# Kernel tuning notes

Hardware: AMD Instinct MI355X
Metric: run time of the kernel (lower is better)

## Reference

```python
import jax, jax.numpy as jnp
import numpy as np

B, H, W = 4, 128, 128
D_MODEL = 256
N_LAYERS = 4
N_STATE = 64


def _s4d_kernel(log_dt, logA_re, A_im, C_re, C_im, L):
    """S4D (diagonal SSM) convolution kernel of length L. Shapes: log_dt (d,), others (d,N). Returns (d, L)."""
    dt = jnp.exp(log_dt)                       # (d,)
    A = -jnp.exp(logA_re) + 1j * A_im          # (d,N) complex, Re<0 for stability
    C = C_re + 1j * C_im                       # (d,N)
    dtA = dt[:, None] * A                      # (d,N)
    # ZOH-style input matrix folded into C (S4D-Lin):  C * (exp(dt*A)-1)/A
    CB = C * (jnp.exp(dtA) - 1.0) / A          # (d,N)
    pows = jnp.exp(dtA[:, :, None] * jnp.arange(L, dtype=jnp.float32))  # (d,N,L)
    K = jnp.einsum('dn,dnl->dl', CB, pows)     # (d,L) complex
    return 2.0 * K.real


def _layernorm(x, w, b, eps=1e-5):
    mu = jnp.mean(x, axis=-1, keepdims=True)
    var = jnp.mean(jnp.square(x - mu), axis=-1, keepdims=True)
    return (x - mu) * jax.lax.rsqrt(var + eps) * w + b


def setup_inputs() -> dict:
    key = jax.random.key(0)
    ks = jax.random.split(key, 16)
    d, L, N = D_MODEL, N_LAYERS, N_STATE
    x = jax.random.normal(ks[0], (B, H, W, 1), dtype=jnp.float32)
    grid = jax.random.uniform(ks[1], (B, H, W, 1), dtype=jnp.float32)
    W_enc = jax.random.normal(ks[2], (2, d), dtype=jnp.float32) / np.sqrt(2.0)
    b_enc = jnp.zeros((d,), jnp.float32)
    # per-layer, per-axis (axis 0 = H-kernel, axis 1 = W-kernel) SSM params
    log_dt = jax.random.uniform(ks[3], (L, 2, d), jnp.float32,
                                minval=float(np.log(1e-3)), maxval=float(np.log(1e-1)))
    logA_re = jnp.full((L, 2, d, N), float(np.log(0.5)), jnp.float32)
    A_im = jnp.broadcast_to(np.pi * jnp.arange(N, dtype=jnp.float32), (L, 2, d, N)).copy()
    C_re = jax.random.normal(ks[4], (L, 2, d, N), jnp.float32) * float(0.5 ** 0.5)
    C_im = jax.random.normal(ks[5], (L, 2, d, N), jnp.float32) * float(0.5 ** 0.5)
    Dskip = jax.random.normal(ks[6], (L, d), jnp.float32)
    W_out = jax.random.normal(ks[7], (L, d, 2 * d), jnp.float32) / np.sqrt(d)
    b_out = jnp.zeros((L, 2 * d), jnp.float32)
    ln_w = jnp.ones((L, d), jnp.float32)
    ln_b = jnp.zeros((L, d), jnp.float32)
    W_dec = jax.random.normal(ks[8], (d, 1), jnp.float32) / np.sqrt(d)
    b_dec = jnp.zeros((1,), jnp.float32)
    return dict(x=x, grid=grid, W_enc=W_enc, b_enc=b_enc, log_dt=log_dt,
                logA_re=logA_re, A_im=A_im, C_re=C_re, C_im=C_im, Dskip=Dskip,
                W_out=W_out, b_out=b_out, ln_w=ln_w, ln_b=ln_b, W_dec=W_dec, b_dec=b_dec)


def reference(x, grid, W_enc, b_enc, log_dt, logA_re, A_im, C_re, C_im,
              Dskip, W_out, b_out, ln_w, ln_b, W_dec, b_dec):
    # encoder: concat grid, project to d_model  -> (B,H,W,d)
    h = jnp.concatenate([x, grid], axis=-1) @ W_enc + b_enc
    n_fft = (2 * H, 2 * W)
    for i in range(N_LAYERS):
        z = h
        # separable 2D S4ND kernel: outer product of per-axis S4D kernels
        kh = _s4d_kernel(log_dt[i, 0], logA_re[i, 0], A_im[i, 0], C_re[i, 0], C_im[i, 0], H)  # (d,H)
        kw = _s4d_kernel(log_dt[i, 1], logA_re[i, 1], A_im[i, 1], C_re[i, 1], C_im[i, 1], W)  # (d,W)
        K2 = kh[:, :, None] * kw[:, None, :]                     # (d,H,W)
        u = jnp.transpose(z, (0, 3, 1, 2))                       # (B,d,H,W)
        yf = jnp.fft.rfft2(u, s=n_fft) * jnp.fft.rfft2(K2, s=n_fft)
        y = jnp.fft.irfft2(yf, s=n_fft)[..., :H, :W]             # causal 2D conv via zero-pad FFT
        y = y + u * Dskip[i][:, None, None]                      # skip connection D*u
        y = jnp.transpose(y, (0, 2, 3, 1))                       # back to (B,H,W,d)
        y = jax.nn.gelu(y)
        y = y @ W_out[i] + b_out[i]                              # (B,H,W,2d)
        a, g = jnp.split(y, 2, axis=-1)
        y = a * jax.nn.sigmoid(g)                                # GLU output linear
        h = y + h                                                # residual (dropout=0, eval)
        h = _layernorm(h, ln_w[i], ln_b[i])                      # post-norm (prenorm=False)
    return h @ W_dec + b_dec                                     # (B,H,W,1)
```

## Files before the change

kernel.cpp:

```cpp
#include <hip/hip_runtime.h>
#include <math.h>

#define DM 256
#define NS 64
#define SP 128

typedef __attribute__((ext_vector_type(8))) short bf16x8;
typedef __attribute__((ext_vector_type(4))) float f32x4;

__device__ __forceinline__ float gelu_f(float x) {
    float x3 = x * x * x;
    return 0.5f * x * (1.0f + tanhf(0.7978845608028654f * (x + 0.044715f * x3)));
}
__device__ __forceinline__ float sigmoid_f(float x) {
    return 1.0f / (1.0f + expf(-x));
}
__device__ __forceinline__ unsigned short f2bf(float f) {
    unsigned u = __float_as_uint(f);
    u += 0x7fff + ((u >> 16) & 1);
    return (unsigned short)(u >> 16);
}
__device__ __forceinline__ float bf2f(unsigned short b) {
    return __uint_as_float(((unsigned)b) << 16);
}

__global__ __launch_bounds__(128) void gen_k_kernel(
        const float* __restrict__ log_dt, const float* __restrict__ logA_re,
        const float* __restrict__ A_im,   const float* __restrict__ C_re,
        const float* __restrict__ C_im,   float* __restrict__ Kd) {
    int blk = blockIdx.x;
    int d  = blk & (DM - 1);
    int la = blk >> 8;
    int q  = threadIdx.x;
    __shared__ float s_cbr[NS], s_cbi[NS], s_dr[NS], s_di[NS];
    int pbase = (la * DM + d) * NS;
    float dt = expf(log_dt[la * DM + d]);
    if (q < NS) {
        int n = q;
        float ar = -expf(logA_re[pbase + n]);
        float ai = A_im[pbase + n];
        float dr = dt * ar, di = dt * ai;
        float er = expf(dr);
        float sn, cs;
        sincosf(di, &sn, &cs);
        float nr = er * cs - 1.0f, ni = er * sn;
        float inv = 1.0f / (ar * ar + ai * ai);
        float br = (nr * ar + ni * ai) * inv;
        float bi = (ni * ar - nr * ai) * inv;
        float cr = C_re[pbase + n], ci = C_im[pbase + n];
        s_cbr[n] = cr * br - ci * bi;
        s_cbi[n] = cr * bi + ci * br;
        s_dr[n] = dr;
        s_di[n] = di;
    }
    __syncthreads();
    float fq = (float)q;
    float acc = 0.0f;
    for (int n = 0; n < NS; ++n) {
        float pr = expf(s_dr[n] * fq);
        float sn, cs;
        sincosf(s_di[n] * fq, &sn, &cs);
        acc += s_cbr[n] * (pr * cs) - s_cbi[n] * (pr * sn);
    }
    Kd[((size_t)la * DM + d) * SP + q] = 2.0f * acc;
}

__global__ __launch_bounds__(256) void toep_kernel(
        const float* __restrict__ Kd, unsigned short* __restrict__ Tp, int l) {
    int blk = blockIdx.x;
    int axis = blk >> 8, d = blk & 255;
    int la = l * 2 + axis;
    __shared__ float kt[SP];
    if (threadIdx.x < SP) kt[threadIdx.x] = Kd[((size_t)la * DM + d) * SP + threadIdx.x];
    __syncthreads();
    size_t bse = ((size_t)axis * DM + d) * 16384;
    for (int e = threadIdx.x; e < 16384; e += 256) {
        int i = e >> 7, j = e & 127;
        Tp[bse + e] = (j <= i) ? f2bf(kt[i - j]) : (unsigned short)0;
    }
}

__global__ __launch_bounds__(256) void prep_b_kernel(
        const float* __restrict__ Wo, unsigned short* __restrict__ Bt) {
    int idx = blockIdx.x * 256 + threadIdx.x;
    int l = idx >> 17, rem = idx & 131071, n = rem >> 8, k = rem & 255;
    Bt[idx] = f2bf(Wo[(size_t)l * 131072 + k * 512 + n]);
}

__global__ __launch_bounds__(256) void encode_kernel(
        const float* __restrict__ x, const float* __restrict__ g,
        const float* __restrict__ W_enc, const float* __restrict__ b_enc,
        unsigned short* __restrict__ h) {
    int total = 4 * SP * SP * 128;
    for (int idx = blockIdx.x * blockDim.x + threadIdx.x; idx < total;
         idx += gridDim.x * blockDim.x) {
        int c = (idx & 127) * 2;
        int pos = idx >> 7;
        float xv = x[pos], gv = g[pos];
        float v0 = xv * W_enc[c] + gv * W_enc[DM + c] + b_enc[c];
        float v1 = xv * W_enc[c + 1] + gv * W_enc[DM + c + 1] + b_enc[c + 1];
        unsigned o = (unsigned)f2bf(v0) | ((unsigned)f2bf(v1) << 16);
        *(unsigned*)(h + (size_t)pos * DM + c) = o;
    }
}

template <int FUSE>
__global__ __launch_bounds__(256) void transpose_kernel(
        const unsigned short* __restrict__ in, unsigned short* __restrict__ out,
        int Ci, int Ri, int ctmask, int ctshift,
        const unsigned short* __restrict__ hres, const float* __restrict__ Dsk) {
    __shared__ unsigned tile[64][65];
    int bid = blockIdx.x;
    int rt = bid >> ctshift, ct = bid & ctmask;
    int r0 = rt << 6, c0 = ct << 6;
    int tid = threadIdx.x;
    #pragma unroll
    for (int rep = 0; rep < 2; ++rep) {
        int e = rep * 256 + tid;
        int p = e >> 3, cc = e & 7;
        uint4 v = *(const uint4*)(in + (size_t)(r0 + p) * Ci + c0 + cc * 8);
        const unsigned short* pv = (const unsigned short*)&v;
        #pragma unroll
        for (int q = 0; q < 8; ++q) tile[p][cc * 8 + q] = pv[q];
    }
    __syncthreads();
    #pragma unroll
    for (int rep = 0; rep < 2; ++rep) {
        int e = rep * 256 + tid;
        int cc = e >> 3, pc = e & 7;
        unsigned short tmp[8];
        #pragma unroll
        for (int q = 0; q < 8; ++q) tmp[q] = (unsigned short)tile[pc * 8 + q][cc];
        size_t oaddr = (size_t)(c0 + cc) * Ri + r0 + pc * 8;
        if (FUSE) {
            int d0 = r0 + pc * 8;
            uint4 hv = *(const uint4*)(hres + oaddr);
            const unsigned short* hvp = (const unsigned short*)&hv;
            float4 dk0 = *(const float4*)(Dsk + d0);
            float4 dk1 = *(const float4*)(Dsk + d0 + 4);
            #pragma unroll
            for (int q = 0; q < 8; ++q) {
                float dk = (q < 4) ? (&dk0.x)[q] : (&dk1.x)[q - 4];
                float z = fmaf(bf2f(hvp[q]), dk, bf2f(tmp[q]));
                tmp[q] = f2bf(gelu_f(z));
            }
        }
        *(uint4*)(out + oaddr) = *(const uint4*)tmp;
    }
}

__global__ __launch_bounds__(512, 4) void conv_kernel(
        const unsigned short* __restrict__ hc, const unsigned short* __restrict__ Tp,
        unsigned short* __restrict__ Zc) {
    __shared__ unsigned short Tile[128][128];
    __shared__ unsigned short TpL[128][128];
    int bid = blockIdx.x;
    int work = (bid & 7) * 128 + (bid >> 3);
    int d = work >> 2, b = work & 3;
    int tid = threadIdx.x;
    int lane = tid & 63, wv = tid >> 6;
    int lc = lane & 15, g = lane >> 4;

    const unsigned short* TpW = Tp + (size_t)(DM + d) * 16384;
    const unsigned short* TpH = Tp + (size_t)d * 16384;

    {
        const uint4* srcU = (const uint4*)(hc + ((size_t)d * 4 + b) * 16384);
        const uint4* srcT = (const uint4*)TpW;
        #pragma unroll
        for (int it = 0; it < 4; ++it) {
            int e = it * 512 + tid;
            int r = e >> 4, wc = e & 15;
            *(uint4*)&Tile[r][((wc ^ (r & 7)) << 3)] = srcU[e];
            *(uint4*)&TpL[r][((wc ^ (r & 7)) << 3)] = srcT[e];
        }
    }
    __syncthreads();

    f32x4 acc[8];
    #pragma unroll
    for (int ni = 0; ni < 8; ++ni) acc[ni] = (f32x4){0.f, 0.f, 0.f, 0.f};
    #pragma unroll
    for (int kk = 0; kk < 4; ++kk) {
        int hh = wv * 16 + lc;
        bf16x8 a = *(const bf16x8*)&Tile[hh][(((kk * 4 + g) ^ (hh & 7)) << 3)];
        #pragma unroll
        for (int ni = 0; ni < 8; ++ni) {
            int n = ni * 16 + lc;
            bf16x8 bf = *(const bf16x8*)&TpL[n][(((kk * 4 + g) ^ (n & 7)) << 3)];
            acc[ni] = __builtin_amdgcn_mfma_f32_16x16x32_bf16(a, bf, acc[ni], 0, 0, 0);
        }
    }
    __syncthreads();

    {
        int hh0 = wv * 16 + g * 4;
        #pragma unroll
        for (int ni = 0; ni < 8; ++ni) {
            int w = ni * 16 + lc;
            ushort4 p;
            p.x = f2bf(acc[ni][0]); p.y = f2bf(acc[ni][1]);
            p.z = f2bf(acc[ni][2]); p.w = f2bf(acc[ni][3]);
            *(ushort4*)&Tile[w][((((hh0 >> 3) ^ (w & 7)) << 3) | (hh0 & 7))] = p;
        }
        const uint4* srcT = (const uint4*)TpH;
        #pragma unroll
        for (int it = 0; it < 4; ++it) {
            int e = it * 512 + tid;
            int r = e >> 4, wc = e & 15;
            *(uint4*)&TpL[r][((wc ^ (r & 7)) << 3)] = srcT[e];
        }
    }
    __syncthreads();

    #pragma unroll
    for (int ni = 0; ni < 8; ++ni) acc[ni] = (f32x4){0.f, 0.f, 0.f, 0.f};
    #pragma unroll
    for (int kk = 0; kk < 4; ++kk) {
        int w = wv * 16 + lc;
        bf16x8 a = *(const bf16x8*)&Tile[w][(((kk * 4 + g) ^ (w & 7)) << 3)];
        #pragma unroll
        for (int ni = 0; ni < 8; ++ni) {
            int n = ni * 16 + lc;
            bf16x8 bf = *(const bf16x8*)&TpL[n][(((kk * 4 + g) ^ (n & 7)) << 3)];
            acc[ni] = __builtin_amdgcn_mfma_f32_16x16x32_bf16(a, bf, acc[ni], 0, 0, 0);
        }
    }
    __syncthreads();

    {
        int w0 = wv * 16 + g * 4;
        #pragma unroll
        for (int ni = 0; ni < 8; ++ni) {
            int hh = ni * 16 + lc;
            ushort4 p;
            p.x = f2bf(acc[ni][0]); p.y = f2bf(acc[ni][1]);
            p.z = f2bf(acc[ni][2]); p.w = f2bf(acc[ni][3]);
            *(ushort4*)&Tile[hh][((((w0 >> 3) ^ (hh & 7)) << 3) | (w0 & 7))] = p;
        }
    }
    __syncthreads();
    {
        uint4* dst = (uint4*)(Zc + ((size_t)d * 4 + b) * 16384);
        #pragma unroll
        for (int it = 0; it < 4; ++it) {
            int e = it * 512 + tid;
            int r = e >> 4, wc = e & 15;
            dst[e] = *(const uint4*)&Tile[r][((wc ^ (r & 7)) << 3)];
        }
    }
}

__global__ __launch_bounds__(512, 4) void glu_kernel(
        const unsigned short* __restrict__ Ab, const unsigned short* __restrict__ Bt,
        unsigned short* __restrict__ h, const float* __restrict__ bo) {
    __shared__ unsigned short Ba[64][256];
    __shared__ unsigned short Bg[64][256];
    int tid = threadIdx.x;
    int lane = tid & 63, wv = tid >> 6;
    int lc = lane & 15, g = lane >> 4;
    int mb = blockIdx.x & 127;
    int qp = blockIdx.x >> 7;

    {
        const uint4* srcA = (const uint4*)(Bt + (size_t)(qp * 64) * DM);
        const uint4* srcG = (const uint4*)(Bt + (size_t)(256 + qp * 64) * DM);
        #pragma unroll
        for (int it = 0; it < 4; ++it) {
            int e = it * 512 + tid;
            int r = e >> 5, wc = e & 31;
            *(uint4*)&Ba[r][((wc ^ (r & 7)) << 3)] = srcA[e];
            *(uint4*)&Bg[r][((wc ^ (r & 7)) << 3)] = srcG[e];
        }
    }
    __syncthreads();

    #pragma unroll
    for (int s4 = 0; s4 < 4; ++s4) {
        int mrow = mb * 512 + s4 * 128 + wv * 16 + lc;
        bf16x8 af[8];
        #pragma unroll
        for (int kk = 0; kk < 8; ++kk)
            af[kk] = *(const bf16x8*)(Ab + (size_t)mrow * DM + kk * 32 + g * 8);

        f32x4 aa[4], ag[4];
        #pragma unroll
        for (int ni = 0; ni < 4; ++ni) {
            aa[ni] = (f32x4){0.f, 0.f, 0.f, 0.f};
            ag[ni] = (f32x4){0.f, 0.f, 0.f, 0.f};
        }
        #pragma unroll
        for (int kk = 0; kk < 8; ++kk) {
            #pragma unroll
            for (int ni = 0; ni < 4; ++ni) {
                int r = ni * 16 + lc;
                int ch = (((kk * 4 + g) ^ (r & 7)) << 3);
                bf16x8 bfa = *(const bf16x8*)&Ba[r][ch];
                bf16x8 bfg = *(const bf16x8*)&Bg[r][ch];
                aa[ni] = __builtin_amdgcn_mfma_f32_16x16x32_bf16(bfa, af[kk], aa[ni], 0, 0, 0);
                ag[ni] = __builtin_amdgcn_mfma_f32_16x16x32_bf16(bfg, af[kk], ag[ni], 0, 0, 0);
            }
        }

        #pragma unroll
        for (int ni = 0; ni < 4; ++ni) {
            int ca = qp * 64 + ni * 16 + g * 4;
            float4 bav = *(const float4*)(bo + ca);
            float4 bgv = *(const float4*)(bo + 256 + ca);
            size_t pbase = (size_t)mrow * DM + ca;
            uint2 hv = *(const uint2*)(h + pbase);
            float hr[4];
            hr[0] = __uint_as_float(hv.x << 16);
            hr[1] = __uint_as_float(hv.x & 0xffff0000u);
            hr[2] = __uint_as_float(hv.y << 16);
            hr[3] = __uint_as_float(hv.y & 0xffff0000u);
            float o[4];
            #pragma unroll
            for (int reg = 0; reg < 4; ++reg)
                o[reg] = (aa[ni][reg] + (&bav.x)[reg]) * sigmoid_f(ag[ni][reg] + (&bgv.x)[reg]) + hr[reg];
            uint2 ov;
            ov.x = (unsigned)f2bf(o[0]) | ((unsigned)f2bf(o[1]) << 16);
            ov.y = (unsigned)f2bf(o[2]) | ((unsigned)f2bf(o[3]) << 16);
            *(uint2*)(h + pbase) = ov;
        }
    }
}

__global__ __launch_bounds__(256) void ln_tr_kernel(
        unsigned short* __restrict__ hio, unsigned short* __restrict__ hc,
        const float* __restrict__ lnw, const float* __restrict__ lnb) {
    __shared__ unsigned tile[64][65];
    __shared__ float rs[64][2];
    int r0 = blockIdx.x * 64;
    int tid = threadIdx.x;
    int wv = tid >> 6, lane = tid & 63;

    for (int it = 0; it < 16; ++it) {
        int p = it * 4 + wv;
        size_t base = (size_t)(r0 + p) * DM + lane * 4;
        uint2 hv = *(const uint2*)(hio + base);
        float v0 = __uint_as_float(hv.x << 16);
        float v1 = __uint_as_float(hv.x & 0xffff0000u);
        float v2 = __uint_as_float(hv.y << 16);
        float v3 = __uint_as_float(hv.y & 0xffff0000u);
        float s1 = v0 + v1 + v2 + v3;
        float s2 = v0 * v0 + v1 * v1 + v2 * v2 + v3 * v3;
        #pragma unroll
        for (int off = 1; off < 64; off <<= 1) {
            s1 += __shfl_xor(s1, off);
            s2 += __shfl_xor(s2, off);
        }
        if (lane == 0) {
            float mean = s1 * (1.0f / 256.0f);
            float var = s2 * (1.0f / 256.0f) - mean * mean;
            rs[p][0] = mean;
            rs[p][1] = rsqrtf(var + 1e-5f);
        }
    }
    __syncthreads();

    for (int ct = 0; ct < 4; ++ct) {
        int c0 = ct * 64;
        #pragma unroll
        for (int rep = 0; rep < 2; ++rep) {
            int e = rep * 256 + tid;
            int p = e >> 3, cc = e & 7;
            size_t addr = (size_t)(r0 + p) * DM + c0 + cc * 8;
            uint4 v = *(const uint4*)(hio + addr);
            const unsigned short* vp = (const unsigned short*)&v;
            float mn = rs[p][0], iv = rs[p][1];
            int cb = c0 + cc * 8;
            float4 w0 = *(const float4*)(lnw + cb);
            float4 w1 = *(const float4*)(lnw + cb + 4);
            float4 b0 = *(const float4*)(lnb + cb);
            float4 b1 = *(const float4*)(lnb + cb + 4);
            unsigned short tmp[8];
            #pragma unroll
            for (int q = 0; q < 8; ++q) {
                float lw = (q < 4) ? (&w0.x)[q] : (&w1.x)[q - 4];
                float lb = (q < 4) ? (&b0.x)[q] : (&b1.x)[q - 4];
                tmp[q] = f2bf((bf2f(vp[q]) - mn) * iv * lw + lb);
            }
            *(uint4*)(hio + addr) = *(const uint4*)tmp;
            #pragma unroll
            for (int q = 0; q < 8; ++q) tile[p][cc * 8 + q] = tmp[q];
        }
        __syncthreads();
        #pragma unroll
        for (int rep = 0; rep < 2; ++rep) {
            int e = rep * 256 + tid;
            int cc = e >> 3, pc = e & 7;
            unsigned short tmp[8];
            #pragma unroll
            for (int q = 0; q < 8; ++q) tmp[q] = (unsigned short)tile[pc * 8 + q][cc];
            *(uint4*)(hc + (size_t)(c0 + cc) * 65536 + r0 + pc * 8) = *(const uint4*)tmp;
        }
        __syncthreads();
    }
}

__global__ __launch_bounds__(256) void decode_kernel(
        const unsigned short* __restrict__ h, const float* __restrict__ Wd,
        const float* __restrict__ bd, float* __restrict__ out) {
    int pos = blockIdx.x * 4 + (threadIdx.x >> 6);
    int lane = threadIdx.x & 63;
    float s = 0.0f;
    #pragma unroll
    for (int j = 0; j < 4; ++j) {
        int d = j * 64 + lane;
        s += bf2f(h[(size_t)pos * DM + d]) * Wd[d];
    }
    #pragma unroll
    for (int off = 32; off > 0; off >>= 1) s += __shfl_down(s, off);
    if (lane == 0) out[pos] = s + bd[0];
}

extern "C" void kernel_launch(void* const* d_in, const int* in_sizes, int n_in,
                              void* d_out, int out_size, void* d_ws, size_t ws_size,
                              hipStream_t stream) {
    const float* x       = (const float*)d_in[0];
    const float* grid    = (const float*)d_in[1];
    const float* W_enc   = (const float*)d_in[2];
    const float* b_enc   = (const float*)d_in[3];
    const float* log_dt  = (const float*)d_in[4];
    const float* logA_re = (const float*)d_in[5];
    const float* A_im    = (const float*)d_in[6];
    const float* C_re    = (const float*)d_in[7];
    const float* C_im    = (const float*)d_in[8];
    const float* Dskip   = (const float*)d_in[9];
    const float* W_out   = (const float*)d_in[10];
    const float* b_out   = (const float*)d_in[11];
    const float* ln_w    = (const float*)d_in[12];
    const float* ln_b    = (const float*)d_in[13];
    const float* W_dec   = (const float*)d_in[14];
    const float* b_dec   = (const float*)d_in[15];

    char* base = (char*)d_ws;
    float*          Kd  = (float*)base;
    unsigned short* Bt  = (unsigned short*)(base + 1048576);
    unsigned short* hP  = (unsigned short*)(base + 2097152);
    unsigned short* R1  = (unsigned short*)(base + 35651584);
    unsigned short* R2  = (unsigned short*)(base + 69206016);
    unsigned short* Tp  = (unsigned short*)(base + 102760448);

    gen_k_kernel<<<dim3(8 * DM), dim3(128), 0, stream>>>(log_dt, logA_re, A_im,
                                                         C_re, C_im, Kd);
    prep_b_kernel<<<dim3(2048), dim3(256), 0, stream>>>(W_out, Bt);
    encode_kernel<<<dim3(2048), dim3(256), 0, stream>>>(x, grid, W_enc, b_enc, hP);
    transpose_kernel<0><<<dim3(4096), dim3(256), 0, stream>>>(
        hP, R1, 256, 65536, 3, 2, (const unsigned short*)nullptr, (const float*)nullptr);

    for (int l = 0; l < 4; ++l) {
        toep_kernel<<<dim3(512), dim3(256), 0, stream>>>(Kd, Tp, l);
        conv_kernel<<<dim3(1024), dim3(512), 0, stream>>>(R1, Tp, R2);
        transpose_kernel<1><<<dim3(4096), dim3(256), 0, stream>>>(
            R2, R1, 65536, 256, 1023, 10, hP, Dskip + (size_t)l * DM);
        glu_kernel<<<dim3(512), dim3(512), 0, stream>>>(R1,
            Bt + (size_t)l * 131072, hP, b_out + (size_t)l * 512);
        ln_tr_kernel<<<dim3(1024), dim3(256), 0, stream>>>(hP, R1,
            ln_w + (size_t)l * DM, ln_b + (size_t)l * DM);
    }

    decode_kernel<<<dim3(16384), dim3(256), 0, stream>>>(hP, W_dec, b_dec,
                                                         (float*)d_out);
}
```

Baseline: 533.3 us.

## Build Toeplitz tiles in-kernel from Kd and skip last-layer transposed write

Measured after the change: 524.4 us. About the same (-1.7%).

```diff
diff --git a/kernel.cpp b/kernel.cpp
--- a/kernel.cpp
+++ b/kernel.cpp
@@ -65,21 +65,6 @@
     Kd[((size_t)la * DM + d) * SP + q] = 2.0f * acc;
 }
 
-__global__ __launch_bounds__(256) void toep_kernel(
-        const float* __restrict__ Kd, unsigned short* __restrict__ Tp, int l) {
-    int blk = blockIdx.x;
-    int axis = blk >> 8, d = blk & 255;
-    int la = l * 2 + axis;
-    __shared__ float kt[SP];
-    if (threadIdx.x < SP) kt[threadIdx.x] = Kd[((size_t)la * DM + d) * SP + threadIdx.x];
-    __syncthreads();
-    size_t bse = ((size_t)axis * DM + d) * 16384;
-    for (int e = threadIdx.x; e < 16384; e += 256) {
-        int i = e >> 7, j = e & 127;
-        Tp[bse + e] = (j <= i) ? f2bf(kt[i - j]) : (unsigned short)0;
-    }
-}
-
 __global__ __launch_bounds__(256) void prep_b_kernel(
         const float* __restrict__ Wo, unsigned short* __restrict__ Bt) {
     int idx = blockIdx.x * 256 + threadIdx.x;
@@ -150,10 +135,11 @@
 }
 
 __global__ __launch_bounds__(512, 4) void conv_kernel(
-        const unsigned short* __restrict__ hc, const unsigned short* __restrict__ Tp,
-        unsigned short* __restrict__ Zc) {
+        const unsigned short* __restrict__ hc, const float* __restrict__ Kd,
+        int l, unsigned short* __restrict__ Zc) {
     __shared__ unsigned short Tile[128][128];
     __shared__ unsigned short TpL[128][128];
+    __shared__ float ktw[SP], kth[SP];
     int bid = blockIdx.x;
     int work = (bid & 7) * 128 + (bid >> 3);
     int d = work >> 2, b = work & 3;
@@ -161,18 +147,28 @@
     int lane = tid & 63, wv = tid >> 6;
     int lc = lane & 15, g = lane >> 4;
 
-    const unsigned short* TpW = Tp + (size_t)(DM + d) * 16384;
-    const unsigned short* TpH = Tp + (size_t)d * 16384;
-
     {
         const uint4* srcU = (const uint4*)(hc + ((size_t)d * 4 + b) * 16384);
-        const uint4* srcT = (const uint4*)TpW;
         #pragma unroll
         for (int it = 0; it < 4; ++it) {
             int e = it * 512 + tid;
             int r = e >> 4, wc = e & 15;
             *(uint4*)&Tile[r][((wc ^ (r & 7)) << 3)] = srcU[e];
-            *(uint4*)&TpL[r][((wc ^ (r & 7)) << 3)] = srcT[e];
+        }
+        if (tid < 128)
+            ktw[tid] = Kd[((size_t)(l * 2 + 1) * DM + d) * SP + tid];
+        else if (tid < 256)
+            kth[tid - 128] = Kd[((size_t)(l * 2 + 0) * DM + d) * SP + tid - 128];
+    }
+    __syncthreads();
+
+    {
+        int c = tid & 127, rb = tid >> 7;
+        #pragma unroll
+        for (int it = 0; it < 32; ++it) {
+            int r = it * 4 + rb;
+            unsigned short v = (c <= r) ? f2bf(ktw[r - c]) : (unsigned short)0;
+            TpL[r][(((c >> 3) ^ (r & 7)) << 3) | (c & 7)] = v;
         }
     }
     __syncthreads();
@@ -203,12 +199,12 @@
             p.z = f2bf(acc[ni][2]); p.w = f2bf(acc[ni][3]);
             *(ushort4*)&Tile[w][((((hh0 >> 3) ^ (w & 7)) << 3) | (hh0 & 7))] = p;
         }
-        const uint4* srcT = (const uint4*)TpH;
-        #pragma unroll
-        for (int it = 0; it < 4; ++it) {
-            int e = it * 512 + tid;
-            int r = e >> 4, wc = e & 15;
-            *(uint4*)&TpL[r][((wc ^ (r & 7)) << 3)] = srcT[e];
+        int c = tid & 127, rb = tid >> 7;
+        #pragma unroll
+        for (int it = 0; it < 32; ++it) {
+            int r = it * 4 + rb;
+            unsigned short v = (c <= r) ? f2bf(kth[r - c]) : (unsigned short)0;
+            TpL[r][(((c >> 3) ^ (r & 7)) << 3) | (c & 7)] = v;
         }
     }
     __syncthreads();
@@ -326,6 +322,7 @@
     }
 }
 
+template <int WRITE_HC>
 __global__ __launch_bounds__(256) void ln_tr_kernel(
         unsigned short* __restrict__ hio, unsigned short* __restrict__ hc,
         const float* __restrict__ lnw, const float* __restrict__ lnb) {
@@ -382,20 +379,24 @@
                 tmp[q] = f2bf((bf2f(vp[q]) - mn) * iv * lw + lb);
             }
             *(uint4*)(hio + addr) = *(const uint4*)tmp;
+            if (WRITE_HC) {
+                #pragma unroll
+                for (int q = 0; q < 8; ++q) tile[p][cc * 8 + q] = tmp[q];
+            }
+        }
+        if (WRITE_HC) {
+            __syncthreads();
             #pragma unroll
-            for (int q = 0; q < 8; ++q) tile[p][cc * 8 + q] = tmp[q];
-        }
-        __syncthreads();
-        #pragma unroll
-        for (int rep = 0; rep < 2; ++rep) {
-            int e = rep * 256 + tid;
-            int cc = e >> 3, pc = e & 7;
-            unsigned short tmp[8];
-            #pragma unroll
-            for (int q = 0; q < 8; ++q) tmp[q] = (unsigned short)tile[pc * 8 + q][cc];
-            *(uint4*)(hc + (size_t)(c0 + cc) * 65536 + r0 + pc * 8) = *(const uint4*)tmp;
-        }
-        __syncthreads();
+            for (int rep = 0; rep < 2; ++rep) {
+                int e = rep * 256 + tid;
+                int cc = e >> 3, pc = e & 7;
+                unsigned short tmp[8];
+                #pragma unroll
+                for (int q = 0; q < 8; ++q) tmp[q] = (unsigned short)tile[pc * 8 + q][cc];
+                *(uint4*)(hc + (size_t)(c0 + cc) * 65536 + r0 + pc * 8) = *(const uint4*)tmp;
+            }
+            __syncthreads();
+        }
     }
 }
 
@@ -441,7 +442,6 @@
     unsigned short* hP  = (unsigned short*)(base + 2097152);
     unsigned short* R1  = (unsigned short*)(base + 35651584);
     unsigned short* R2  = (unsigned short*)(base + 69206016);
-    unsigned short* Tp  = (unsigned short*)(base + 102760448);
 
     gen_k_kernel<<<dim3(8 * DM), dim3(128), 0, stream>>>(log_dt, logA_re, A_im,
                                                          C_re, C_im, Kd);
@@ -451,14 +451,17 @@
         hP, R1, 256, 65536, 3, 2, (const unsigned short*)nullptr, (const float*)nullptr);
 
     for (int l = 0; l < 4; ++l) {
-        toep_kernel<<<dim3(512), dim3(256), 0, stream>>>(Kd, Tp, l);
-        conv_kernel<<<dim3(1024), dim3(512), 0, stream>>>(R1, Tp, R2);
+        conv_kernel<<<dim3(1024), dim3(512), 0, stream>>>(R1, Kd, l, R2);
         transpose_kernel<1><<<dim3(4096), dim3(256), 0, stream>>>(
             R2, R1, 65536, 256, 1023, 10, hP, Dskip + (size_t)l * DM);
         glu_kernel<<<dim3(512), dim3(512), 0, stream>>>(R1,
             Bt + (size_t)l * 131072, hP, b_out + (size_t)l * 512);
-        ln_tr_kernel<<<dim3(1024), dim3(256), 0, stream>>>(hP, R1,
-            ln_w + (size_t)l * DM, ln_b + (size_t)l * DM);
+        if (l < 3)
+            ln_tr_kernel<1><<<dim3(1024), dim3(256), 0, stream>>>(hP, R1,
+                ln_w + (size_t)l * DM, ln_b + (size_t)l * DM);
+        else
+            ln_tr_kernel<0><<<dim3(1024), dim3(256), 0, stream>>>(hP, R1,
+                ln_w + (size_t)l * DM, ln_b + (size_t)l * DM);
     }
 
     decode_kernel<<<dim3(16384), dim3(256), 0, stream>>>(hP, W_dec, b_dec,
```
